# Optimization experiments

Hardware: AMD Instinct MI355X
Metric: run time of the kernel (lower is better)

Reference implementation:

```python
import jax, jax.numpy as jnp
import numpy as np

LAYER_LAYOUT = [64, 128, 128, 128, 10]
B, D, D_OUT, L_GNN = 16, 128, 10, 3
N = sum(LAYER_LAYOUT)            # 458 nodes per graph


def _build_edge_index():
    # nn_to_edge_index: fully-connected bipartite edges between consecutive layers
    offs = np.cumsum([0] + LAYER_LAYOUT)
    src, dst = [], []
    for i in range(1, len(LAYER_LAYOUT)):
        s = np.arange(offs[i - 1], offs[i])
        d = np.arange(offs[i], offs[i + 1])
        ss, dd = np.meshgrid(s, d, indexing='ij')
        src.append(ss.ravel())
        dst.append(dd.ravel())
    return np.stack([np.concatenate(src), np.concatenate(dst)])  # [2, E]


def setup_inputs() -> dict:
    key = jax.random.key(0)
    ks = jax.random.split(key, 8)
    E = 42240
    edge_index = jnp.asarray(_build_edge_index(), dtype=jnp.int64)
    return {
        'node_features': jax.random.normal(ks[0], (B, N, D), jnp.float32),
        'edge_attr': jax.random.normal(ks[1], (B, E, D), jnp.float32),
        'w_msg': jax.random.normal(ks[2], (L_GNN, 3 * D, D), jnp.float32) / jnp.sqrt(3.0 * D),
        'b_msg': jnp.zeros((L_GNN, D), jnp.float32),
        'w_self': jax.random.normal(ks[3], (L_GNN, D, D), jnp.float32) / jnp.sqrt(1.0 * D),
        'b_self': jnp.zeros((L_GNN, D), jnp.float32),
        'w1': jax.random.normal(ks[4], (D, D), jnp.float32) / jnp.sqrt(1.0 * D),
        'b1': jnp.zeros((D,), jnp.float32),
        'w2': jax.random.normal(ks[5], (D, D), jnp.float32) / jnp.sqrt(1.0 * D),
        'b2': jnp.zeros((D,), jnp.float32),
        'w3': jax.random.normal(ks[6], (D, D_OUT), jnp.float32) / jnp.sqrt(1.0 * D),
        'b3': jnp.zeros((D_OUT,), jnp.float32),
        'edge_index': edge_index,
    }


def reference(node_features, edge_attr, w_msg, b_msg, w_self, b_self,
              w1, b1, w2, b2, w3, b3, edge_index):
    src, dst = edge_index[0], edge_index[1]
    E = src.shape[0]
    # in-degree per destination node (shared across the batch)
    deg = jax.ops.segment_sum(jnp.ones((E,), node_features.dtype), dst, num_segments=N)
    denom = jnp.maximum(deg, 1.0)[:, None]  # [N, 1]

    def aggregate(m):  # m: [B, E, D] -> [B, N, D] mean over incoming edges
        return jax.vmap(lambda mm: jax.ops.segment_sum(mm, dst, num_segments=N))(m) / denom

    x = node_features
    for l in range(L_GNN):
        # edge message: relu(W [x_src, x_dst, e])
        m = jnp.concatenate([x[:, src], x[:, dst], edge_attr], axis=-1)  # [B, E, 3D]
        m = jax.nn.relu(jnp.einsum('bef,fd->bed', m, w_msg[l]) + b_msg[l])
        agg = aggregate(m)  # [B, N, D]
        x = jax.nn.relu(jnp.einsum('bnf,fd->bnd', x, w_self[l]) + b_self[l] + agg)

    # graph_features == 'mean' over nodes, then proj_out MLP head
    g = x.mean(axis=1)  # [B, D]
    h = jax.nn.relu(g @ w1 + b1)
    h = jax.nn.relu(h @ w2 + b2)
    return h @ w3 + b3  # [B, D_OUT]
```

## Files before the change

kernel.cpp:

```cpp
#include <hip/hip_runtime.h>
#include <hip/hip_bf16.h>

#define D 128
#define NNODES 458
#define BATCH 16
#define ETOT 42240
#define LGNN 3
#define ESPLITS 2

typedef __bf16 bf16x8 __attribute__((ext_vector_type(8)));
typedef float f32x4 __attribute__((ext_vector_type(4)));

__device__ inline bf16x8 cvt8v(f32x4 a, f32x4 b) {
    bf16x8 r;
    r[0] = (__bf16)a[0]; r[1] = (__bf16)a[1]; r[2] = (__bf16)a[2]; r[3] = (__bf16)a[3];
    r[4] = (__bf16)b[0]; r[5] = (__bf16)b[1]; r[6] = (__bf16)b[2]; r[7] = (__bf16)b[3];
    return r;
}

__global__ __launch_bounds__(256) void cvt_edge_kernel(
    const f32x4* __restrict__ src, bf16x8* __restrict__ dst)
{
    const size_t total = (size_t)BATCH * ETOT * (D / 8);
    size_t i = (size_t)blockIdx.x * 256 + threadIdx.x;
    const size_t stride = (size_t)gridDim.x * 256;
    for (; i < total; i += stride) {
        f32x4 a = __builtin_nontemporal_load(&src[2 * i]);
        f32x4 b = __builtin_nontemporal_load(&src[2 * i + 1]);
        dst[i] = cvt8v(a, b);
    }
}

__global__ __launch_bounds__(256) void wt_kernel(
    const float* __restrict__ w_msg, __bf16* __restrict__ wT)
{
    const int l = blockIdx.x;
    const float* w3s = w_msg + (size_t)l * 384 * 128 + 256 * 128;
    __bf16* wTl = wT + (size_t)l * 128 * 128;
    for (int idx = threadIdx.x; idx < 128 * 128; idx += 256) {
        int n = idx >> 7, k = idx & 127;
        wTl[idx] = (__bf16)w3s[k * 128 + n];
    }
}

__global__ __launch_bounds__(256) void node_proj_kernel(
    const float* __restrict__ x,
    const float* __restrict__ wmsg_l,
    const float* __restrict__ bmsg_l,
    const float* __restrict__ wself_l,
    const float* __restrict__ bself_l,
    float* __restrict__ asrc, float* __restrict__ bdst, float* __restrict__ xs)
{
    const int b     = blockIdx.y;
    const int n0    = blockIdx.x * 16;
    const int which = blockIdx.z;
    const int tid   = threadIdx.x;

    __shared__ float xt[16 * D];
    for (int i = tid; i < 16 * D; i += 256) {
        int r = i >> 7;
        int n = n0 + r; if (n >= NNODES) n = NNODES - 1;
        xt[i] = x[((size_t)b * NNODES + n) * D + (i & 127)];
    }
    __syncthreads();

    const int d    = tid & 127;
    const int half = tid >> 7;

    const float* w = (which == 0) ? wmsg_l
                   : (which == 1) ? (wmsg_l + D * D)
                                  : wself_l;

    float acc[8] = {};
    for (int k = 0; k < D; ++k) {
        float wv = w[k * D + d];
#pragma unroll
        for (int r = 0; r < 8; ++r)
            acc[r] += xt[(half * 8 + r) * D + k] * wv;
    }

    const float bias = (which == 1) ? bmsg_l[d] : (which == 2) ? bself_l[d] : 0.f;
    float* outp = (which == 0) ? asrc : (which == 1) ? bdst : xs;
#pragma unroll
    for (int r = 0; r < 8; ++r) {
        int n = n0 + half * 8 + r;
        if (n < NNODES) {
            size_t o = ((size_t)b * NNODES + n) * D + d;
            outp[o] = acc[r] + bias;
        }
    }
}

__global__ __launch_bounds__(256) void edge_kernel(
    const bf16x8* __restrict__ eb,
    const __bf16* __restrict__ wT_l,
    const float* __restrict__ asrc,
    const float* __restrict__ bdst,
    float* __restrict__ aggp)
{
    const int tile  = blockIdx.x;
    const int b     = blockIdx.y;
    const int split = blockIdx.z;

    int j0, Nsrc, Ndst, e_off, src_off, dst_off;
    if (tile < 8)       { j0 = tile * 16;        Nsrc = 64;  Ndst = 128; e_off = 0;     src_off = 0;   dst_off = 64;  }
    else if (tile < 16) { j0 = (tile - 8) * 16;  Nsrc = 128; Ndst = 128; e_off = 8192;  src_off = 64;  dst_off = 192; }
    else if (tile < 24) { j0 = (tile - 16) * 16; Nsrc = 128; Ndst = 128; e_off = 24576; src_off = 192; dst_off = 320; }
    else                { j0 = 0;                Nsrc = 128; Ndst = 10;  e_off = 40960; src_off = 320; dst_off = 448; }

    const int chunk = Nsrc / ESPLITS;
    const int s0    = split * chunk;

    const int tid  = threadIdx.x;
    const int wave = tid >> 6;
    const int lane = tid & 63;
    const int lm   = lane & 15;
    const int q    = lane >> 4;

    bf16x8 bfrag[2][4];
#pragma unroll
    for (int t = 0; t < 2; ++t) {
        int n = wave * 32 + t * 16 + lm;
#pragma unroll
        for (int kk = 0; kk < 4; ++kk)
            bfrag[t][kk] = *(const bf16x8*)(wT_l + n * 128 + kk * 32 + q * 8);
    }

    float bpv[2][4];
#pragma unroll
    for (int t = 0; t < 2; ++t)
#pragma unroll
        for (int r = 0; r < 4; ++r) {
            int j = j0 + q * 4 + r; if (j > Ndst - 1) j = Ndst - 1;
            bpv[t][r] = bdst[((size_t)b * NNODES + dst_off + j) * D + wave * 32 + t * 16 + lm];
        }

    int m_eff = (j0 + lm < Ndst) ? lm : (Ndst - 1 - j0);
    const bf16x8* ap = eb +
        ((size_t)b * ETOT + e_off + (size_t)s0 * Ndst + j0 + m_eff) * 16 + q;
    const float* as_ptr = asrc + ((size_t)b * NNODES + src_off + s0) * D;

    float acc[2][4] = {};
#pragma unroll 4
    for (int s = 0; s < chunk; ++s) {
        bf16x8 afrag[4];
#pragma unroll
        for (int kk = 0; kk < 4; ++kk) afrag[kk] = ap[kk * 4];
        float as0 = as_ptr[wave * 32 + lm];
        float as1 = as_ptr[wave * 32 + 16 + lm];
        ap += Ndst * 16;
        as_ptr += D;

#pragma unroll
        for (int t = 0; t < 2; ++t) {
            f32x4 c = {0.f, 0.f, 0.f, 0.f};
#pragma unroll
            for (int kk = 0; kk < 4; ++kk)
                c = __builtin_amdgcn_mfma_f32_16x16x32_bf16(afrag[kk], bfrag[t][kk], c, 0, 0, 0);
            float as_d = t ? as1 : as0;
#pragma unroll
            for (int r = 0; r < 4; ++r) {
                float v = c[r] + as_d + bpv[t][r];
                acc[t][r] += fmaxf(v, 0.f);
            }
        }
    }

    const float inv_deg = 1.0f / (float)Nsrc;
    float* aout = aggp + (size_t)split * BATCH * NNODES * D;
#pragma unroll
    for (int t = 0; t < 2; ++t)
#pragma unroll
        for (int r = 0; r < 4; ++r) {
            int j = j0 + q * 4 + r;
            if (j < Ndst)
                aout[((size_t)b * NNODES + dst_off + j) * D + wave * 32 + t * 16 + lm] =
                    acc[t][r] * inv_deg;
        }
}

__global__ __launch_bounds__(256) void update_kernel(
    const float4* __restrict__ xs,
    const float4* __restrict__ agg0, const float4* __restrict__ agg1,
    float4* __restrict__ x)
{
    int i = blockIdx.x * 256 + threadIdx.x;
    int rowi = i >> 5;
    int n = rowi % NNODES;
    float4 v = xs[i];
    if (n >= 64) {
        float4 a = agg0[i], c = agg1[i];
        v.x += a.x + c.x; v.y += a.y + c.y; v.z += a.z + c.z; v.w += a.w + c.w;
    }
    v.x = fmaxf(v.x, 0.f); v.y = fmaxf(v.y, 0.f);
    v.z = fmaxf(v.z, 0.f); v.w = fmaxf(v.w, 0.f);
    x[i] = v;
}

__global__ __launch_bounds__(256) void head_kernel(
    const float* __restrict__ x,
    const float* __restrict__ w1, const float* __restrict__ b1,
    const float* __restrict__ w2, const float* __restrict__ b2,
    const float* __restrict__ w3, const float* __restrict__ b3,
    float* __restrict__ out)
{
    const int b = blockIdx.x;
    const int tid = threadIdx.x;
    __shared__ float tmp[256];
    __shared__ float g[128], h1[128], h2[128];

    const int d = tid & 127, half = tid >> 7;
    float s = 0.f;
    for (int n = half; n < NNODES; n += 2)
        s += x[((size_t)b * NNODES + n) * D + d];
    tmp[tid] = s;
    __syncthreads();
    if (tid < 128) g[tid] = (tmp[tid] + tmp[tid + 128]) * (1.0f / (float)NNODES);
    __syncthreads();

    if (tid < 128) {
        float a = 0.f;
        for (int k = 0; k < D; ++k) a += g[k] * w1[k * D + tid];
        h1[tid] = fmaxf(a + b1[tid], 0.f);
    }
    __syncthreads();
    if (tid < 128) {
        float a = 0.f;
        for (int k = 0; k < D; ++k) a += h1[k] * w2[k * D + tid];
        h2[tid] = fmaxf(a + b2[tid], 0.f);
    }
    __syncthreads();
    if (tid < 10) {
        float a = 0.f;
        for (int k = 0; k < D; ++k) a += h2[k] * w3[k * 10 + tid];
        out[b * 10 + tid] = a + b3[tid];
    }
}

extern "C" void kernel_launch(void* const* d_in, const int* in_sizes, int n_in,
                              void* d_out, int out_size, void* d_ws, size_t ws_size,
                              hipStream_t stream) {
    const float* node_features = (const float*)d_in[0];
    const float* edge_attr     = (const float*)d_in[1];
    const float* w_msg         = (const float*)d_in[2];
    const float* b_msg         = (const float*)d_in[3];
    const float* w_self        = (const float*)d_in[4];
    const float* b_self        = (const float*)d_in[5];
    const float* w1 = (const float*)d_in[6];
    const float* b1 = (const float*)d_in[7];
    const float* w2 = (const float*)d_in[8];
    const float* b2 = (const float*)d_in[9];
    const float* w3 = (const float*)d_in[10];
    const float* b3 = (const float*)d_in[11];
    float* out = (float*)d_out;

    float* ws = (float*)d_ws;
    const size_t SZ = (size_t)BATCH * NNODES * D;
    float* x_ws = ws;
    float* asrc = ws + SZ;
    float* bdst = ws + 2 * SZ;
    float* xs   = ws + 3 * SZ;
    float* aggp = ws + 4 * SZ;
    bf16x8* eb  = (bf16x8*)(ws + 6 * SZ);
    __bf16* wT  = (__bf16*)(ws + 6 * SZ + (size_t)BATCH * ETOT * (D / 2));

    cvt_edge_kernel<<<dim3(2048), 256, 0, stream>>>((const f32x4*)edge_attr, eb);
    wt_kernel<<<dim3(3), 256, 0, stream>>>(w_msg, wT);

    for (int l = 0; l < LGNN; ++l) {
        const float* xin    = (l == 0) ? node_features : x_ws;
        const float* wmsg_l = w_msg + (size_t)l * 384 * 128;
        node_proj_kernel<<<dim3(29, 16, 3), 256, 0, stream>>>(
            xin, wmsg_l, b_msg + l * 128, w_self + (size_t)l * 128 * 128,
            b_self + l * 128, asrc, bdst, xs);
        edge_kernel<<<dim3(25, 16, ESPLITS), 256, 0, stream>>>(
            eb, wT + (size_t)l * 128 * 128, asrc, bdst, aggp);
        update_kernel<<<dim3(916), 256, 0, stream>>>(
            (const float4*)xs, (const float4*)aggp,
            (const float4*)(aggp + SZ), (float4*)x_ws);
    }
    head_kernel<<<dim3(16), 256, 0, stream>>>(x_ws, w1, b1, w2, b2, w3, b3, out);
}
```

Before: 971.0 us.

## Split edge work eight ways and fold the node update into projection and head

The edge kernel's source dimension is now split into eight parts instead of two, which gives many more blocks to fill the GPU. The update kernel is removed: the next layer's node-projection kernel, and the head kernel after the last layer, sum the partial aggregates and apply the ReLU when they load x. The three projection GEMMs now run in a single block that shares one x tile, and the edge loop handles two source nodes per iteration to expose more MFMA and load parallelism. In exchange, the partial-aggregate buffer grows, so each consumer reads eight partials per node, and the register pressure in the edge loop goes up.

```diff
diff --git a/kernel.cpp b/kernel.cpp
--- a/kernel.cpp
+++ b/kernel.cpp
@@ -6,7 +6,7 @@
 #define BATCH 16
 #define ETOT 42240
 #define LGNN 3
-#define ESPLITS 2
+#define ESPLITS 8
 
 typedef __bf16 bf16x8 __attribute__((ext_vector_type(8)));
 typedef float f32x4 __attribute__((ext_vector_type(4)));
@@ -44,49 +44,64 @@
 }
 
 __global__ __launch_bounds__(256) void node_proj_kernel(
-    const float* __restrict__ x,
-    const float* __restrict__ wmsg_l,
-    const float* __restrict__ bmsg_l,
-    const float* __restrict__ wself_l,
-    const float* __restrict__ bself_l,
-    float* __restrict__ asrc, float* __restrict__ bdst, float* __restrict__ xs)
-{
-    const int b     = blockIdx.y;
-    const int n0    = blockIdx.x * 16;
-    const int which = blockIdx.z;
-    const int tid   = threadIdx.x;
+    const float* xsrc, const float* __restrict__ aggp, const int mode,
+    const float* __restrict__ wmsg_l, const float* __restrict__ bmsg_l,
+    const float* __restrict__ wself_l, const float* __restrict__ bself_l,
+    float* __restrict__ asrc, float* __restrict__ bdst, float* xs_out)
+{
+    const int b  = blockIdx.y;
+    const int n0 = blockIdx.x * 16;
+    const int tid = threadIdx.x;
 
     __shared__ float xt[16 * D];
-    for (int i = tid; i < 16 * D; i += 256) {
-        int r = i >> 7;
+    const size_t SZ4 = (size_t)BATCH * NNODES * (D / 4);
+    const float4* x4 = (const float4*)xsrc;
+    const float4* a4 = (const float4*)aggp;
+    for (int i4 = tid; i4 < 512; i4 += 256) {
+        int r = i4 >> 5;
         int n = n0 + r; if (n >= NNODES) n = NNODES - 1;
-        xt[i] = x[((size_t)b * NNODES + n) * D + (i & 127)];
+        size_t o = ((size_t)b * NNODES + n) * 32 + (i4 & 31);
+        float4 v = x4[o];
+        if (mode) {
+            if (n >= 64) {
+#pragma unroll
+                for (int p = 0; p < ESPLITS; ++p) {
+                    float4 a = a4[(size_t)p * SZ4 + o];
+                    v.x += a.x; v.y += a.y; v.z += a.z; v.w += a.w;
+                }
+            }
+            v.x = fmaxf(v.x, 0.f); v.y = fmaxf(v.y, 0.f);
+            v.z = fmaxf(v.z, 0.f); v.w = fmaxf(v.w, 0.f);
+        }
+        ((float4*)xt)[i4] = v;
     }
     __syncthreads();
 
     const int d    = tid & 127;
     const int half = tid >> 7;
 
-    const float* w = (which == 0) ? wmsg_l
-                   : (which == 1) ? (wmsg_l + D * D)
-                                  : wself_l;
-
-    float acc[8] = {};
+    float acc0[8] = {}, acc1[8] = {}, acc2[8] = {};
     for (int k = 0; k < D; ++k) {
-        float wv = w[k * D + d];
-#pragma unroll
-        for (int r = 0; r < 8; ++r)
-            acc[r] += xt[(half * 8 + r) * D + k] * wv;
-    }
-
-    const float bias = (which == 1) ? bmsg_l[d] : (which == 2) ? bself_l[d] : 0.f;
-    float* outp = (which == 0) ? asrc : (which == 1) ? bdst : xs;
+        float w1v = wmsg_l[k * D + d];
+        float w2v = wmsg_l[(D + k) * D + d];
+        float wsv = wself_l[k * D + d];
+#pragma unroll
+        for (int r = 0; r < 8; ++r) {
+            float xv = xt[(half * 8 + r) * D + k];
+            acc0[r] += xv * w1v;
+            acc1[r] += xv * w2v;
+            acc2[r] += xv * wsv;
+        }
+    }
+    const float bm = bmsg_l[d], bs = bself_l[d];
 #pragma unroll
     for (int r = 0; r < 8; ++r) {
         int n = n0 + half * 8 + r;
         if (n < NNODES) {
             size_t o = ((size_t)b * NNODES + n) * D + d;
-            outp[o] = acc[r] + bias;
+            asrc[o]   = acc0[r];
+            bdst[o]   = acc1[r] + bm;
+            xs_out[o] = acc2[r] + bs;
         }
     }
 }
@@ -141,27 +156,36 @@
     const float* as_ptr = asrc + ((size_t)b * NNODES + src_off + s0) * D;
 
     float acc[2][4] = {};
-#pragma unroll 4
-    for (int s = 0; s < chunk; ++s) {
-        bf16x8 afrag[4];
-#pragma unroll
-        for (int kk = 0; kk < 4; ++kk) afrag[kk] = ap[kk * 4];
-        float as0 = as_ptr[wave * 32 + lm];
-        float as1 = as_ptr[wave * 32 + 16 + lm];
-        ap += Ndst * 16;
-        as_ptr += D;
+#pragma unroll 2
+    for (int s = 0; s < chunk; s += 2) {
+        bf16x8 af0[4], af1[4];
+#pragma unroll
+        for (int kk = 0; kk < 4; ++kk) {
+            af0[kk] = ap[kk * 4];
+            af1[kk] = ap[Ndst * 16 + kk * 4];
+        }
+        float a00 = as_ptr[wave * 32 + lm];
+        float a01 = as_ptr[wave * 32 + 16 + lm];
+        float a10 = as_ptr[D + wave * 32 + lm];
+        float a11 = as_ptr[D + wave * 32 + 16 + lm];
+        ap += Ndst * 32;
+        as_ptr += 2 * D;
 
 #pragma unroll
         for (int t = 0; t < 2; ++t) {
-            f32x4 c = {0.f, 0.f, 0.f, 0.f};
-#pragma unroll
-            for (int kk = 0; kk < 4; ++kk)
-                c = __builtin_amdgcn_mfma_f32_16x16x32_bf16(afrag[kk], bfrag[t][kk], c, 0, 0, 0);
-            float as_d = t ? as1 : as0;
+            f32x4 c0 = {0.f, 0.f, 0.f, 0.f};
+            f32x4 c1 = {0.f, 0.f, 0.f, 0.f};
+#pragma unroll
+            for (int kk = 0; kk < 4; ++kk) {
+                c0 = __builtin_amdgcn_mfma_f32_16x16x32_bf16(af0[kk], bfrag[t][kk], c0, 0, 0, 0);
+                c1 = __builtin_amdgcn_mfma_f32_16x16x32_bf16(af1[kk], bfrag[t][kk], c1, 0, 0, 0);
+            }
+            float b0 = t ? a01 : a00;
+            float b1 = t ? a11 : a10;
 #pragma unroll
             for (int r = 0; r < 4; ++r) {
-                float v = c[r] + as_d + bpv[t][r];
-                acc[t][r] += fmaxf(v, 0.f);
+                acc[t][r] += fmaxf(c0[r] + b0 + bpv[t][r], 0.f)
+                           + fmaxf(c1[r] + b1 + bpv[t][r], 0.f);
             }
         }
     }
@@ -179,26 +203,8 @@
         }
 }
 
-__global__ __launch_bounds__(256) void update_kernel(
-    const float4* __restrict__ xs,
-    const float4* __restrict__ agg0, const float4* __restrict__ agg1,
-    float4* __restrict__ x)
-{
-    int i = blockIdx.x * 256 + threadIdx.x;
-    int rowi = i >> 5;
-    int n = rowi % NNODES;
-    float4 v = xs[i];
-    if (n >= 64) {
-        float4 a = agg0[i], c = agg1[i];
-        v.x += a.x + c.x; v.y += a.y + c.y; v.z += a.z + c.z; v.w += a.w + c.w;
-    }
-    v.x = fmaxf(v.x, 0.f); v.y = fmaxf(v.y, 0.f);
-    v.z = fmaxf(v.z, 0.f); v.w = fmaxf(v.w, 0.f);
-    x[i] = v;
-}
-
 __global__ __launch_bounds__(256) void head_kernel(
-    const float* __restrict__ x,
+    const float* __restrict__ xs, const float* __restrict__ aggp,
     const float* __restrict__ w1, const float* __restrict__ b1,
     const float* __restrict__ w2, const float* __restrict__ b2,
     const float* __restrict__ w3, const float* __restrict__ b3,
@@ -208,11 +214,19 @@
     const int tid = threadIdx.x;
     __shared__ float tmp[256];
     __shared__ float g[128], h1[128], h2[128];
+    const size_t SZ = (size_t)BATCH * NNODES * D;
 
     const int d = tid & 127, half = tid >> 7;
     float s = 0.f;
-    for (int n = half; n < NNODES; n += 2)
-        s += x[((size_t)b * NNODES + n) * D + d];
+    for (int n = half; n < NNODES; n += 2) {
+        size_t o = ((size_t)b * NNODES + n) * D + d;
+        float v = xs[o];
+        if (n >= 64) {
+#pragma unroll
+            for (int p = 0; p < ESPLITS; ++p) v += aggp[(size_t)p * SZ + o];
+        }
+        s += fmaxf(v, 0.f);
+    }
     tmp[tid] = s;
     __syncthreads();
     if (tid < 128) g[tid] = (tmp[tid] + tmp[tid + 128]) * (1.0f / (float)NNODES);
@@ -256,28 +270,26 @@
 
     float* ws = (float*)d_ws;
     const size_t SZ = (size_t)BATCH * NNODES * D;
-    float* x_ws = ws;
-    float* asrc = ws + SZ;
-    float* bdst = ws + 2 * SZ;
-    float* xs   = ws + 3 * SZ;
-    float* aggp = ws + 4 * SZ;
-    bf16x8* eb  = (bf16x8*)(ws + 6 * SZ);
-    __bf16* wT  = (__bf16*)(ws + 6 * SZ + (size_t)BATCH * ETOT * (D / 2));
+    float* asrc = ws;
+    float* bdst = ws + SZ;
+    float* xs   = ws + 2 * SZ;
+    float* aggp = ws + 3 * SZ;
+    bf16x8* eb  = (bf16x8*)(ws + 11 * SZ);
+    __bf16* wT  = (__bf16*)(ws + 11 * SZ + (size_t)BATCH * ETOT * (D / 2));
 
     cvt_edge_kernel<<<dim3(2048), 256, 0, stream>>>((const f32x4*)edge_attr, eb);
     wt_kernel<<<dim3(3), 256, 0, stream>>>(w_msg, wT);
 
     for (int l = 0; l < LGNN; ++l) {
-        const float* xin    = (l == 0) ? node_features : x_ws;
+        const float* xin    = (l == 0) ? node_features : xs;
         const float* wmsg_l = w_msg + (size_t)l * 384 * 128;
-        node_proj_kernel<<<dim3(29, 16, 3), 256, 0, stream>>>(
-            xin, wmsg_l, b_msg + l * 128, w_self + (size_t)l * 128 * 128,
+        node_proj_kernel<<<dim3(29, 16), 256, 0, stream>>>(
+            xin, aggp, (l == 0) ? 0 : 1,
+            wmsg_l, b_msg + l * 128, w_self + (size_t)l * 128 * 128,
             b_self + l * 128, asrc, bdst, xs);
         edge_kernel<<<dim3(25, 16, ESPLITS), 256, 0, stream>>>(
             eb, wT + (size_t)l * 128 * 128, asrc, bdst, aggp);
-        update_kernel<<<dim3(916), 256, 0, stream>>>(
-            (const float4*)xs, (const float4*)aggp,
-            (const float4*)(aggp + SZ), (float4*)x_ws);
-    }
-    head_kernel<<<dim3(16), 256, 0, stream>>>(x_ws, w1, b1, w2, b2, w3, b3, out);
-}
+    }
+    head_kernel<<<dim3(16), 256, 0, stream>>>(
+        xs, aggp, w1, b1, w2, b2, w3, b3, out);
+}
```

Result: no change. 967.5 us (-0.4%).
